# Kernel tuning notes

Measured on AMD Instinct MI355X. Metric: run time of the kernel, lower is better.

Reference implementation:

```python
import jax, jax.numpy as jnp
import numpy as np

TOPK = 16  # module init arg
EPS = 1e-12  # F.normalize eps


def setup_inputs() -> dict:
    key = jax.random.key(0)
    k1, k2, k3 = jax.random.split(key, 3)
    b, c, h, w = 2, 256, 96, 96
    rc = max(c // 4, 16)  # reduced_channels = 64
    x = jax.random.normal(k1, (b, c, h, w), dtype=jnp.float32)
    # 1x1 convs are channel-mixing matmuls; store weights as [out_ch, in_ch]
    w_reduce = jax.random.normal(k2, (rc, c), dtype=jnp.float32) * 0.05
    w_proj = jax.random.normal(k3, (c, rc), dtype=jnp.float32) * 0.05
    return {"x": x, "w_reduce": w_reduce, "w_proj": w_proj}


def reference(x, w_reduce, w_proj):
    b, c, h, w = x.shape
    n = h * w
    # reduce: 1x1 conv == channel matmul -> [b, rc, N]
    feat = jnp.einsum('rc,bchw->brhw', w_reduce, x).reshape(b, -1, n)
    # F.normalize(dim=1): divide by max(L2-norm over channels, eps)
    nrm = jnp.maximum(jnp.sqrt(jnp.sum(feat * feat, axis=1, keepdims=True)), EPS)
    nf = jnp.transpose(feat / nrm, (0, 2, 1))  # [b, N, rc]
    # cosine similarity matrix [b, N, N]
    sim = jnp.einsum('bnr,bmr->bnm', nf, nf)
    k = min(TOPK, n)
    _, idx = jax.lax.top_k(sim, k)  # [b, N, k]
    # gather top-k neighbor features and average -> [b, N, rc]
    corr = jax.vmap(lambda f, i: f[i].mean(axis=1))(nf, idx)
    # proj: 1x1 conv back to C channels, NCHW layout
    enhanced = jnp.einsum('cr,bnr->bnc', w_proj, corr)
    enhanced = jnp.transpose(enhanced, (0, 2, 1)).reshape(b, c, h, w)
    return x + enhanced
```

## Files before the change

### kernel.cpp

```cpp
#include <hip/hip_runtime.h>
#include <cstdint>
#include <cstddef>

#define NPIX 9216
#define NB 2
#define NC 256
#define RC 64
#define TK 16
#define NROWS (NB * NPIX)
#define CT 128
#define ECOLS 1152
#define NTE 9
#define MAXC 128
#define LCAP 64
#define MARGIN 0.008f

typedef unsigned short ushort_t;
typedef unsigned int uint_t;
typedef __bf16 bf16x8 __attribute__((ext_vector_type(8)));
typedef float f32x4 __attribute__((ext_vector_type(4)));

__device__ __forceinline__ uint_t f2bf(float x) {
  uint_t u = __float_as_uint(x);
  return (u + 0x7FFFu + ((u >> 16) & 1u)) >> 16;
}

__device__ __forceinline__ uint_t ordu(float v) {
  uint_t u = __float_as_uint(v);
  return (u & 0x80000000u) ? ~u : (u | 0x80000000u);
}

#define GL2LDS(gsrc, ldst)                                                   \
  __builtin_amdgcn_global_load_lds(                                          \
      (const __attribute__((address_space(1))) uint_t*)(const void*)(gsrc),  \
      (__attribute__((address_space(3))) uint_t*)(void*)(ldst), 16, 0, 0)

__device__ __forceinline__ void stage_tile(
    const ushort_t* __restrict__ nf_hi, size_t cbase, int cb,
    ushort_t* shbuf, int tid) {
  const int wave = tid >> 6, l = tid & 63;
  const int lr = l >> 3;
  const int ls = (l & 7) ^ lr;
#pragma unroll
  for (int i = 0; i < 4; ++i) {
    const int j = wave * 4 + i;
    const ushort_t* g = nf_hi + (cbase + (size_t)(cb + j * 8 + lr)) * 64 + ls * 8;
    ushort_t* d = shbuf + j * 512;
    GL2LDS(g, d);
  }
}

__global__ __launch_bounds__(256) void k_reduce(
    const float* __restrict__ x, const float* __restrict__ wr,
    float* __restrict__ feat4) {
  __shared__ float wl[64 * 16];
  const int bi = blockIdx.x;
  const int pg = bi >> 4, rq = (bi >> 2) & 3, cq = bi & 3;
  const int tid = threadIdx.x;
  {
    const int cl = tid >> 2, rg = (tid & 3) * 4;
#pragma unroll
    for (int i = 0; i < 4; ++i)
      wl[cl * 16 + rg + i] = wr[(size_t)(rq * 16 + rg + i) * NC + cq * 64 + cl];
  }
  __syncthreads();

  const int p = pg * 256 + tid;
  const int b = p >= NPIX;
  const int n = p - b * NPIX;
  const float* xp = x + (size_t)b * NC * NPIX + (size_t)cq * 64 * NPIX + n;

  float4 acc[4];
#pragma unroll
  for (int i = 0; i < 4; ++i) acc[i] = make_float4(0.f, 0.f, 0.f, 0.f);

  for (int c = 0; c < 64; ++c) {
    const float xv = xp[(size_t)c * NPIX];
    const float4* w4 = (const float4*)(wl + c * 16);
#pragma unroll
    for (int i = 0; i < 4; ++i) {
      float4 w = w4[i];
      acc[i].x += w.x * xv; acc[i].y += w.y * xv;
      acc[i].z += w.z * xv; acc[i].w += w.w * xv;
    }
  }
  float4* o = (float4*)(feat4 + (((size_t)(rq * 4 + cq)) * NROWS + p) * 16);
#pragma unroll
  for (int i = 0; i < 4; ++i) o[i] = acc[i];
}

__global__ __launch_bounds__(256) void k_normsplit(
    const float* __restrict__ feat4, float* __restrict__ nf,
    ushort_t* __restrict__ hi) {
  const int t = blockIdx.x * 256 + threadIdx.x;
  const int p = t >> 2, q = t & 3;
  float4 v[4];
#pragma unroll
  for (int i = 0; i < 4; ++i) v[i] = make_float4(0.f, 0.f, 0.f, 0.f);
#pragma unroll
  for (int pt = 0; pt < 4; ++pt) {
    const float4* fp = (const float4*)(feat4 + (((size_t)(q * 4 + pt)) * NROWS + p) * 16);
#pragma unroll
    for (int i = 0; i < 4; ++i) {
      float4 a = fp[i];
      v[i].x += a.x; v[i].y += a.y; v[i].z += a.z; v[i].w += a.w;
    }
  }
  float ssq = 0.f;
#pragma unroll
  for (int i = 0; i < 4; ++i)
    ssq += v[i].x * v[i].x + v[i].y * v[i].y + v[i].z * v[i].z + v[i].w * v[i].w;
  ssq += __shfl_xor(ssq, 1);
  ssq += __shfl_xor(ssq, 2);
  const float inv = 1.f / fmaxf(sqrtf(ssq), 1e-12f);

  float s[16];
#pragma unroll
  for (int i = 0; i < 4; ++i) {
    s[i * 4 + 0] = v[i].x * inv; s[i * 4 + 1] = v[i].y * inv;
    s[i * 4 + 2] = v[i].z * inv; s[i * 4 + 3] = v[i].w * inv;
  }
  float4* no = (float4*)(nf + (size_t)p * RC + q * 16);
#pragma unroll
  for (int i = 0; i < 4; ++i)
    no[i] = make_float4(s[i * 4], s[i * 4 + 1], s[i * 4 + 2], s[i * 4 + 3]);

  uint_t hs[16];
#pragma unroll
  for (int i = 0; i < 16; ++i) hs[i] = f2bf(s[i]);
  uint4* ho = (uint4*)(hi + (size_t)p * RC + q * 16);
#pragma unroll
  for (int h = 0; h < 2; ++h)
    ho[h] = make_uint4(hs[h*8+0] | (hs[h*8+1] << 16), hs[h*8+2] | (hs[h*8+3] << 16),
                       hs[h*8+4] | (hs[h*8+5] << 16), hs[h*8+6] | (hs[h*8+7] << 16));
}

__global__ __launch_bounds__(256) void k_sim_max(
    const ushort_t* __restrict__ nf_hi, float* __restrict__ tmax) {
  __shared__ ushort_t sh[CT * 64];
  const int rb = blockIdx.x >> 3, q = blockIdx.x & 7;
  const int tid = threadIdx.x, wave = tid >> 6, lane = tid & 63;
  const int n = lane & 15, quad = lane >> 4;
  const int r0 = rb * 128 + wave * 32 + n, r1 = r0 + 16;
  const int b = rb >= 72;
  const size_t cbase = (size_t)b * NPIX;
  const int x0 = (quad ^ (n & 7)) * 8;
  const int x1 = ((quad + 4) ^ (n & 7)) * 8;

  const bf16x8 bh00 = *(const bf16x8*)(nf_hi + (size_t)r0 * 64 + quad * 8);
  const bf16x8 bh01 = *(const bf16x8*)(nf_hi + (size_t)r0 * 64 + 32 + quad * 8);
  const bf16x8 bh10 = *(const bf16x8*)(nf_hi + (size_t)r1 * 64 + quad * 8);
  const bf16x8 bh11 = *(const bf16x8*)(nf_hi + (size_t)r1 * 64 + 32 + quad * 8);

  float cm0 = -1e30f, cm1 = -1e30f;

  for (int t = 0; t < NTE; ++t) {
    stage_tile(nf_hi, cbase, q * ECOLS + t * CT, sh, tid);
    __syncthreads();

#pragma unroll
    for (int st = 0; st < 8; ++st) {
      const ushort_t* ap = sh + (st * 16 + n) * 64;
      bf16x8 ah0 = *(const bf16x8*)(ap + x0);
      bf16x8 ah1 = *(const bf16x8*)(ap + x1);
      f32x4 z = {0.f, 0.f, 0.f, 0.f};
      f32x4 a0 = __builtin_amdgcn_mfma_f32_16x16x32_bf16(ah0, bh00, z, 0, 0, 0);
      a0 = __builtin_amdgcn_mfma_f32_16x16x32_bf16(ah1, bh01, a0, 0, 0, 0);
      f32x4 a1 = __builtin_amdgcn_mfma_f32_16x16x32_bf16(ah0, bh10, z, 0, 0, 0);
      a1 = __builtin_amdgcn_mfma_f32_16x16x32_bf16(ah1, bh11, a1, 0, 0, 0);
      cm0 = fmaxf(fmaxf(a0[0], a0[1]), fmaxf(fmaxf(a0[2], a0[3]), cm0));
      cm1 = fmaxf(fmaxf(a1[0], a1[1]), fmaxf(fmaxf(a1[2], a1[3]), cm1));
    }
    if (t % 3 == 2) {
      const int cn = t / 3;
      tmax[(size_t)r0 * 96 + (q * 4 + quad) * 3 + cn] = cm0;
      tmax[(size_t)r1 * 96 + (q * 4 + quad) * 3 + cn] = cm1;
      cm0 = -1e30f; cm1 = -1e30f;
    }
    __syncthreads();
  }
}

__global__ __launch_bounds__(256) void k_thresh(
    const float* __restrict__ tmax, float* __restrict__ Tb) {
  const int wave = threadIdx.x >> 6, lane = threadIdx.x & 63;
  const int row = blockIdx.x * 4 + wave;
  const float* tp = tmax + (size_t)row * 96;
  float v0 = tp[lane];
  float v1 = (lane < 32) ? tp[64 + lane] : -1e30f;
  float m = -1e30f;
#pragma unroll
  for (int k = 0; k < TK; ++k) {
    float c = fmaxf(v0, v1);
#pragma unroll
    for (int d = 1; d < 64; d <<= 1) c = fmaxf(c, __shfl_xor(c, d));
    m = c;
    if (v0 == m) v0 = -1e30f;
    if (v1 == m) v1 = -1e30f;
  }
  if (lane == 0) Tb[row] = m - MARGIN;
}

__global__ __launch_bounds__(256) void k_collect(
    const ushort_t* __restrict__ nf_hi, const float* __restrict__ Tb,
    int* __restrict__ cidx, int* __restrict__ rowcnt) {
  __shared__ ushort_t sh[CT * 64];
  __shared__ ushort_t lst[128][LCAP + 1];
  __shared__ int lcnt[128];
  const int rb = blockIdx.x >> 3, q = blockIdx.x & 7;
  const int tid = threadIdx.x, wave = tid >> 6, lane = tid & 63;
  const int n = lane & 15, quad = lane >> 4;
  const int rl0 = wave * 32 + n, rl1 = rl0 + 16;
  const int r0 = rb * 128 + rl0, r1 = r0 + 16;
  const int b = rb >= 72;
  const size_t cbase = (size_t)b * NPIX;
  const int x0 = (quad ^ (n & 7)) * 8;
  const int x1 = ((quad + 4) ^ (n & 7)) * 8;

  if (tid < 128) lcnt[tid] = 0;

  const bf16x8 bh00 = *(const bf16x8*)(nf_hi + (size_t)r0 * 64 + quad * 8);
  const bf16x8 bh01 = *(const bf16x8*)(nf_hi + (size_t)r0 * 64 + 32 + quad * 8);
  const bf16x8 bh10 = *(const bf16x8*)(nf_hi + (size_t)r1 * 64 + quad * 8);
  const bf16x8 bh11 = *(const bf16x8*)(nf_hi + (size_t)r1 * 64 + 32 + quad * 8);

  const float T0 = Tb[r0], T1 = Tb[r1];

  for (int t = 0; t < NTE; ++t) {
    const int cb = q * ECOLS + t * CT;
    stage_tile(nf_hi, cbase, cb, sh, tid);
    __syncthreads();

#pragma unroll
    for (int st = 0; st < 8; ++st) {
      const ushort_t* ap = sh + (st * 16 + n) * 64;
      bf16x8 ah0 = *(const bf16x8*)(ap + x0);
      bf16x8 ah1 = *(const bf16x8*)(ap + x1);
      f32x4 z = {0.f, 0.f, 0.f, 0.f};
      f32x4 a0 = __builtin_amdgcn_mfma_f32_16x16x32_bf16(ah0, bh00, z, 0, 0, 0);
      a0 = __builtin_amdgcn_mfma_f32_16x16x32_bf16(ah1, bh01, a0, 0, 0, 0);
      f32x4 a1 = __builtin_amdgcn_mfma_f32_16x16x32_bf16(ah0, bh10, z, 0, 0, 0);
      a1 = __builtin_amdgcn_mfma_f32_16x16x32_bf16(ah1, bh11, a1, 0, 0, 0);

      const int c0 = cb + st * 16 + quad * 4;
      const int m0 = (a0[0] >= T0) | ((a0[1] >= T0) << 1) |
                     ((a0[2] >= T0) << 2) | ((a0[3] >= T0) << 3);
      if (m0) {
        int slot = atomicAdd(&lcnt[rl0], __popc(m0));
#pragma unroll
        for (int r = 0; r < 4; ++r)
          if (m0 & (1 << r)) {
            if (slot < LCAP) lst[rl0][slot] = (ushort_t)(c0 + r);
            ++slot;
          }
      }
      const int m1 = (a1[0] >= T1) | ((a1[1] >= T1) << 1) |
                     ((a1[2] >= T1) << 2) | ((a1[3] >= T1) << 3);
      if (m1) {
        int slot = atomicAdd(&lcnt[rl1], __popc(m1));
#pragma unroll
        for (int r = 0; r < 4; ++r)
          if (m1 & (1 << r)) {
            if (slot < LCAP) lst[rl1][slot] = (ushort_t)(c0 + r);
            ++slot;
          }
      }
    }
    __syncthreads();
  }
  if (tid < 128) {
    const int row = rb * 128 + tid;
    const int cnt = min(lcnt[tid], LCAP);
    int base = atomicAdd(rowcnt + row, cnt);
    for (int j = 0; j < cnt; ++j) {
      const int gs = base + j;
      if (gs < MAXC) cidx[(size_t)row * MAXC + gs] = (int)lst[tid][j];
    }
  }
}

__global__ __launch_bounds__(256) void k_merge_gather(
    const float* __restrict__ nf, const int* __restrict__ cidx,
    const int* __restrict__ rowcnt, float* __restrict__ corr) {
  __shared__ ushort_t selc[4][TK];
  const int wave = threadIdx.x >> 6, lane = threadIdx.x & 63;
  const int row = blockIdx.x * 4 + wave;
  const int b = row >= NPIX;
  const int rl = row - b * NPIX;
  const float* nfb = nf + (size_t)b * NPIX * RC;
  const int C = min(rowcnt[row], MAXC);

  if (lane < TK) selc[wave][lane] = (ushort_t)rl;
  __syncthreads();

  float4 rv[16];
  const float4* r4 = (const float4*)(nf + (size_t)row * RC);
#pragma unroll
  for (int i = 0; i < 16; ++i) rv[i] = r4[i];

  const int* cp = cidx + (size_t)row * MAXC;
  unsigned long long k0 = 0, k1 = 0;
  int c0 = rl, c1 = rl;
  {
    c0 = (lane < C) ? cp[lane] : rl;
    const float4* g = (const float4*)(nfb + (size_t)c0 * RC);
    float s = 0.f;
#pragma unroll
    for (int i = 0; i < 16; ++i) {
      float4 a = g[i];
      s += a.x * rv[i].x + a.y * rv[i].y + a.z * rv[i].z + a.w * rv[i].w;
    }
    if (lane < C)
      k0 = ((unsigned long long)ordu(s) << 32) | (uint_t)(~(uint_t)c0);
  }
  if (C > 64) {
    c1 = (64 + lane < C) ? cp[64 + lane] : rl;
    const float4* g = (const float4*)(nfb + (size_t)c1 * RC);
    float s = 0.f;
#pragma unroll
    for (int i = 0; i < 16; ++i) {
      float4 a = g[i];
      s += a.x * rv[i].x + a.y * rv[i].y + a.z * rv[i].z + a.w * rv[i].w;
    }
    if (64 + lane < C)
      k1 = ((unsigned long long)ordu(s) << 32) | (uint_t)(~(uint_t)c1);
  }

  unsigned long long thr = 0;
#pragma unroll
  for (int bit = 63; bit >= 0; --bit) {
    const unsigned long long cand = thr | (1ull << bit);
    const int cnt = __popcll(__ballot(k0 >= cand)) + __popcll(__ballot(k1 >= cand));
    if (cnt >= TK) thr = cand;
  }
  if (thr != 0) {
    const unsigned long long ml = (lane == 0) ? 0ull : (~0ull >> (64 - lane));
    const unsigned long long b0 = __ballot(k0 >= thr);
    const unsigned long long b1 = __ballot(k1 >= thr);
    const int n0 = __popcll(b0);
    if (k0 >= thr) {
      const int r = __popcll(b0 & ml);
      if (r < TK) selc[wave][r] = (ushort_t)c0;
    }
    if (k1 >= thr) {
      const int r = n0 + __popcll(b1 & ml);
      if (r < TK) selc[wave][r] = (ushort_t)c1;
    }
  }
  __syncthreads();

  float acc = 0.f;
#pragma unroll
  for (int t = 0; t < TK; ++t)
    acc += nfb[(size_t)selc[wave][t] * RC + lane];
  corr[(size_t)row * RC + lane] = acc * 0.0625f;
}

__global__ __launch_bounds__(256) void k_proj_add(
    const float* __restrict__ x, const float* __restrict__ wp,
    const float* __restrict__ corr, float* __restrict__ out) {
  const int pg = blockIdx.x >> 3, cq = blockIdx.x & 7;
  const int tid = threadIdx.x;

  __shared__ float wl[32 * RC];
  {
    const float4* src = (const float4*)(wp + (size_t)cq * 32 * RC);
    float4* dst = (float4*)wl;
#pragma unroll
    for (int i = 0; i < 2; ++i) dst[i * 256 + tid] = src[i * 256 + tid];
  }

  const int p = pg * 256 + tid;
  const int b = p >= NPIX;
  const int n = p - b * NPIX;

  float4 cr[16];
  const float4* c4 = (const float4*)(corr + (size_t)p * RC);
#pragma unroll
  for (int i = 0; i < 16; ++i) cr[i] = c4[i];
  __syncthreads();

  const size_t xb = (size_t)b * NC * NPIX + n;
  for (int cl = 0; cl < 32; ++cl) {
    const float4* w4 = (const float4*)(wl + cl * RC);
    float s = 0.f;
#pragma unroll
    for (int i = 0; i < 16; ++i) {
      float4 w = w4[i];
      s += w.x * cr[i].x + w.y * cr[i].y + w.z * cr[i].z + w.w * cr[i].w;
    }
    const int c = cq * 32 + cl;
    const size_t oi = xb + (size_t)c * NPIX;
    out[oi] = x[oi] + s;
  }
}

extern "C" void kernel_launch(void* const* d_in, const int* in_sizes, int n_in,
                              void* d_out, int out_size, void* d_ws, size_t ws_size,
                              hipStream_t stream) {
  const float* x = (const float*)d_in[0];
  const float* wr = (const float*)d_in[1];
  const float* wp = (const float*)d_in[2];
  float* out = (float*)d_out;

  char* ws = (char*)d_ws;
  float* feat4 = (float*)ws;
  float* tmax = (float*)ws;
  float* corr = (float*)ws;
  float* nf = (float*)(ws + 18874368);
  ushort_t* nf_hi = (ushort_t*)(ws + 23592960);
  float* Tb = (float*)(ws + 25952256);
  int* rowcnt = (int*)(ws + 26025984);
  int* cidx = (int*)(ws + 26099712);

  hipLaunchKernelGGL(k_reduce, dim3(1152), dim3(256), 0, stream, x, wr, feat4);
  hipLaunchKernelGGL(k_normsplit, dim3(288), dim3(256), 0, stream, feat4, nf, nf_hi);
  hipLaunchKernelGGL(k_sim_max, dim3(1152), dim3(256), 0, stream, nf_hi, tmax);
  hipLaunchKernelGGL(k_thresh, dim3(NROWS / 4), dim3(256), 0, stream, tmax, Tb);
  hipMemsetAsync(rowcnt, 0, NROWS * sizeof(int), stream);
  hipLaunchKernelGGL(k_collect, dim3(1152), dim3(256), 0, stream,
                     nf_hi, Tb, cidx, rowcnt);
  hipLaunchKernelGGL(k_merge_gather, dim3(NROWS / 4), dim3(256), 0, stream,
                     nf, cidx, rowcnt, corr);
  hipLaunchKernelGGL(k_proj_add, dim3(576), dim3(256), 0, stream, x, wp, corr, out);
}
```

Baseline: 273.8 us.

## Double-buffer shared-memory tiles in sim_max and collect kernels

Replaces the single shared tile with ping-pong buffers so the next column tile is staged while MFMA work runs on the current one, halving the barriers per tile. The intent is to overlap global loads with compute in both the max-finding and candidate-collection passes. Shared memory per block doubles, which may lower occupancy, particularly in k_collect, which already holds the candidate lists.

```diff
diff --git a/kernel.cpp b/kernel.cpp
--- a/kernel.cpp
+++ b/kernel.cpp
@@ -137,7 +137,8 @@
 
 __global__ __launch_bounds__(256) void k_sim_max(
     const ushort_t* __restrict__ nf_hi, float* __restrict__ tmax) {
-  __shared__ ushort_t sh[CT * 64];
+  __shared__ ushort_t shA[CT * 64];
+  __shared__ ushort_t shB[CT * 64];
   const int rb = blockIdx.x >> 3, q = blockIdx.x & 7;
   const int tid = threadIdx.x, wave = tid >> 6, lane = tid & 63;
   const int n = lane & 15, quad = lane >> 4;
@@ -154,13 +155,10 @@
 
   float cm0 = -1e30f, cm1 = -1e30f;
 
-  for (int t = 0; t < NTE; ++t) {
-    stage_tile(nf_hi, cbase, q * ECOLS + t * CT, sh, tid);
-    __syncthreads();
-
+  auto compute = [&](const ushort_t* shc, int t) {
 #pragma unroll
     for (int st = 0; st < 8; ++st) {
-      const ushort_t* ap = sh + (st * 16 + n) * 64;
+      const ushort_t* ap = shc + (st * 16 + n) * 64;
       bf16x8 ah0 = *(const bf16x8*)(ap + x0);
       bf16x8 ah1 = *(const bf16x8*)(ap + x1);
       f32x4 z = {0.f, 0.f, 0.f, 0.f};
@@ -177,8 +175,20 @@
       tmax[(size_t)r1 * 96 + (q * 4 + quad) * 3 + cn] = cm1;
       cm0 = -1e30f; cm1 = -1e30f;
     }
+  };
+
+  stage_tile(nf_hi, cbase, q * ECOLS, shA, tid);
+  __syncthreads();
+#pragma unroll 1
+  for (int t = 0; t < NTE - 1; t += 2) {
+    stage_tile(nf_hi, cbase, q * ECOLS + (t + 1) * CT, shB, tid);
+    compute(shA, t);
     __syncthreads();
-  }
+    stage_tile(nf_hi, cbase, q * ECOLS + (t + 2) * CT, shA, tid);
+    compute(shB, t + 1);
+    __syncthreads();
+  }
+  compute(shA, NTE - 1);
 }
 
 __global__ __launch_bounds__(256) void k_thresh(
@@ -204,7 +214,8 @@
 __global__ __launch_bounds__(256) void k_collect(
     const ushort_t* __restrict__ nf_hi, const float* __restrict__ Tb,
     int* __restrict__ cidx, int* __restrict__ rowcnt) {
-  __shared__ ushort_t sh[CT * 64];
+  __shared__ ushort_t shA[CT * 64];
+  __shared__ ushort_t shB[CT * 64];
   __shared__ ushort_t lst[128][LCAP + 1];
   __shared__ int lcnt[128];
   const int rb = blockIdx.x >> 3, q = blockIdx.x & 7;
@@ -226,14 +237,11 @@
 
   const float T0 = Tb[r0], T1 = Tb[r1];
 
-  for (int t = 0; t < NTE; ++t) {
+  auto compute = [&](const ushort_t* shc, int t) {
     const int cb = q * ECOLS + t * CT;
-    stage_tile(nf_hi, cbase, cb, sh, tid);
-    __syncthreads();
-
 #pragma unroll
     for (int st = 0; st < 8; ++st) {
-      const ushort_t* ap = sh + (st * 16 + n) * 64;
+      const ushort_t* ap = shc + (st * 16 + n) * 64;
       bf16x8 ah0 = *(const bf16x8*)(ap + x0);
       bf16x8 ah1 = *(const bf16x8*)(ap + x1);
       f32x4 z = {0.f, 0.f, 0.f, 0.f};
@@ -266,8 +274,21 @@
           }
       }
     }
+  };
+
+  stage_tile(nf_hi, cbase, q * ECOLS, shA, tid);
+  __syncthreads();
+#pragma unroll 1
+  for (int t = 0; t < NTE - 1; t += 2) {
+    stage_tile(nf_hi, cbase, q * ECOLS + (t + 1) * CT, shB, tid);
+    compute(shA, t);
     __syncthreads();
-  }
+    stage_tile(nf_hi, cbase, q * ECOLS + (t + 2) * CT, shA, tid);
+    compute(shB, t + 1);
+    __syncthreads();
+  }
+  compute(shA, NTE - 1);
+  __syncthreads();
   if (tid < 128) {
     const int row = rb * 128 + tid;
     const int cnt = min(lcnt[tid], LCAP);
```

Measured after the change: 271.6 us. About the same (-0.8%).
